# Kernel tuning notes

Measured on AMD Instinct MI355X. Metric: run time of the kernel, lower is better.

## Reference

```python
import jax, jax.numpy as jnp
import numpy as np

N = 100000   # nodes
E = 800000   # edges
P = 100000   # pos/neg pairs
H = 4        # heads
IN = 128     # input feature dim
HID = 32     # per-head out dim (H*HID = 128)


def gat_layer(h, src, dst, W, al, ar, b):
    """DGL-style GATConv: gather -> leaky_relu attention -> segment softmax -> scatter."""
    n = h.shape[0]
    nh, nf = al.shape
    feat = (h @ W).reshape(n, nh, nf)                       # [N,H,F]
    el = jnp.einsum('nhf,hf->nh', feat, al)                 # [N,H]
    er = jnp.einsum('nhf,hf->nh', feat, ar)                 # [N,H]
    e = jax.nn.leaky_relu(el[src] + er[dst], negative_slope=0.2)  # [E,H]
    emax = jax.ops.segment_max(e, dst, num_segments=n)      # [N,H]
    emax = jnp.where(jnp.isfinite(emax), emax, 0.0)         # zero-in-degree guard
    w = jnp.exp(e - emax[dst])                              # [E,H]
    denom = jax.ops.segment_sum(w, dst, num_segments=n)     # [N,H]
    alpha = w / jnp.maximum(denom[dst], 1e-9)               # [E,H]
    out = jax.ops.segment_sum(feat[src] * alpha[:, :, None], dst, num_segments=n)  # [N,H,F]
    return out.reshape(n, nh * nf) + b


def setup_inputs() -> dict:
    key = jax.random.key(0)
    ks = jax.random.split(key, 32)
    s = 0.1
    d = {
        'x': jax.random.normal(ks[0], (N, IN), jnp.float32),
        'src': jax.random.randint(ks[1], (E,), 0, N),
        'dst': jax.random.randint(ks[2], (E,), 0, N),
        'pos_src': jax.random.randint(ks[3], (P,), 0, N),
        'pos_dst': jax.random.randint(ks[4], (P,), 0, N),
        'neg_src': jax.random.randint(ks[5], (P,), 0, N),
        'neg_dst': jax.random.randint(ks[6], (P,), 0, N),
    }
    HF = H * HID
    # 3 GATConv layers, all 128 -> 4x32
    for l in range(3):
        ind = IN if l == 0 else HF
        d[f'W{l}'] = s * jax.random.normal(ks[7 + 4 * l], (ind, HF), jnp.float32)
        d[f'al{l}'] = s * jax.random.normal(ks[8 + 4 * l], (H, HID), jnp.float32)
        d[f'ar{l}'] = s * jax.random.normal(ks[9 + 4 * l], (H, HID), jnp.float32)
        d[f'b{l}'] = jnp.zeros((HF,), jnp.float32)
    # projection 128 -> 32
    d['Wp'] = s * jax.random.normal(ks[20], (HF, HID), jnp.float32)
    d['bp'] = jnp.zeros((HID,), jnp.float32)
    # predictor MLP 32 -> 32 -> 32 -> 1
    d['Wq1'] = s * jax.random.normal(ks[21], (HID, HID), jnp.float32)
    d['bq1'] = jnp.zeros((HID,), jnp.float32)
    d['Wq2'] = s * jax.random.normal(ks[22], (HID, HID), jnp.float32)
    d['bq2'] = jnp.zeros((HID,), jnp.float32)
    d['Wq3'] = s * jax.random.normal(ks[23], (HID, 1), jnp.float32)
    d['bq3'] = jnp.zeros((1,), jnp.float32)
    return d


def reference(x, src, dst, pos_src, pos_dst, neg_src, neg_dst,
              W0, al0, ar0, b0, W1, al1, ar1, b1, W2, al2, ar2, b2,
              Wp, bp, Wq1, bq1, Wq2, bq2, Wq3, bq3):
    h = x
    for W, al, ar, b in ((W0, al0, ar0, b0), (W1, al1, ar1, b1), (W2, al2, ar2, b2)):
        h = jax.nn.elu(gat_layer(h, src, dst, W, al, ar, b))
    h = h @ Wp + bp                                          # [N,HID]

    def predictor(z):
        z = jax.nn.relu(z @ Wq1 + bq1)
        z = jax.nn.relu(z @ Wq2 + bq2)
        return z @ Wq3 + bq3

    h_pos = predictor(h[pos_src] * h[pos_dst])               # [P,1]
    h_neg = predictor(h[neg_src] * h[neg_dst])               # [P,1]
    return (h_pos, h_neg)
```

## Files before the change

kernel.cpp:

```cpp
#include <hip/hip_runtime.h>
#include <math.h>

typedef __attribute__((ext_vector_type(8))) short bf16x8;
typedef __attribute__((ext_vector_type(4))) float f32x4;

__device__ __forceinline__ unsigned short f2bf_rtne(float v) {
    unsigned u = __float_as_uint(v);
    u += 0x7FFFu + ((u >> 16) & 1u);
    return (unsigned short)(u >> 16);
}

__global__ __launch_bounds__(256) void hist_k(const int* __restrict__ dst, int* __restrict__ deg, int e) {
    int i = blockIdx.x * 256 + threadIdx.x;
    if (i < e) atomicAdd(&deg[dst[i]], 1);
}

__global__ __launch_bounds__(256) void scan1_k(const int* __restrict__ deg, int* __restrict__ rowptr,
                                               int* __restrict__ bsum, int n) {
    __shared__ int sh[256];
    int tid = threadIdx.x;
    int sid = blockIdx.x * 256 + tid;
    int v = (sid < n) ? deg[sid] : 0;
    sh[tid] = v; __syncthreads();
    for (int off = 1; off < 256; off <<= 1) {
        int t = (tid >= off) ? sh[tid - off] : 0;
        __syncthreads();
        sh[tid] += t;
        __syncthreads();
    }
    if (sid < n) rowptr[sid + 1] = sh[tid];
    if (tid == 255) bsum[blockIdx.x] = sh[255];
}

__global__ __launch_bounds__(512) void scan2_k(int* __restrict__ bsum, int nb) {
    __shared__ int sh[512];
    int tid = threadIdx.x;
    sh[tid] = (tid < nb) ? bsum[tid] : 0;
    __syncthreads();
    for (int off = 1; off < 512; off <<= 1) {
        int t = (tid >= off) ? sh[tid - off] : 0;
        __syncthreads();
        sh[tid] += t;
        __syncthreads();
    }
    if (tid < nb) bsum[tid] = sh[tid];
}

__global__ __launch_bounds__(256) void scan3_k(int* __restrict__ rowptr, const int* __restrict__ bsum, int n) {
    int sid = blockIdx.x * 256 + threadIdx.x;
    if (sid == 0) rowptr[0] = 0;
    if (sid < n && blockIdx.x > 0) rowptr[sid + 1] += bsum[blockIdx.x - 1];
}

__global__ __launch_bounds__(256) void fill_k(const int* __restrict__ src, const int* __restrict__ dst,
                                              const int* __restrict__ rowptr, int* __restrict__ cursor,
                                              int* __restrict__ csrc, int* __restrict__ cdst, int e) {
    int i = blockIdx.x * 256 + threadIdx.x;
    if (i < e) {
        int d = dst[i];
        int pos = rowptr[d] + atomicAdd(&cursor[d], 1);
        csrc[pos] = src[i];
        cdst[pos] = d;
    }
}

__global__ __launch_bounds__(256) void wconv_k(const float* __restrict__ W, unsigned short* __restrict__ Bp) {
    int idx = blockIdx.x * 256 + threadIdx.x;
    int k = idx >> 7, nc = idx & 127;
    float v = W[idx];
    unsigned short h = f2bf_rtne(v);
    float hf = __uint_as_float((unsigned)h << 16);
    unsigned short lo = f2bf_rtne(v - hf);
    int n = nc >> 4, l15 = nc & 15, ks = k >> 5, lhi = (k >> 3) & 3, j = k & 7;
    int lanei = lhi * 16 + l15;
    Bp[(((ks * 16 + 2 * n) * 64) + lanei) * 8 + j] = h;
    Bp[(((ks * 16 + 2 * n + 1) * 64) + lanei) * 8 + j] = lo;
}

__global__ __launch_bounds__(256) void gemm_mfma_k(const float* __restrict__ A,
        const unsigned short* __restrict__ Bp,
        const float* __restrict__ alp, const float* __restrict__ arp,
        float* __restrict__ C, float* __restrict__ el, float* __restrict__ er, int M) {
    __shared__ short Bs[4][16][64][8];
    int tid = threadIdx.x;
    int wv = tid >> 6, lane = tid & 63;
    int l15 = lane & 15, lhi = lane >> 4;
    int mb = blockIdx.x * 128 + wv * 32;

    {
        const float4* g = (const float4*)Bp;
        float4* s = (float4*)&Bs[0][0][0][0];
        #pragma unroll
        for (int p = 0; p < 16; p++) s[tid + p * 256] = g[tid + p * 256];
    }

    const float* a0p = A + (size_t)min(mb + l15, M - 1) * 128 + lhi * 8;
    const float* a1p = A + (size_t)min(mb + 16 + l15, M - 1) * 128 + lhi * 8;
    float4 A0[4][2], A1[4][2];
    #pragma unroll
    for (int ks = 0; ks < 4; ks++) {
        A0[ks][0] = *(const float4*)(a0p + ks * 32);
        A0[ks][1] = *(const float4*)(a0p + ks * 32 + 4);
        A1[ks][0] = *(const float4*)(a1p + ks * 32);
        A1[ks][1] = *(const float4*)(a1p + ks * 32 + 4);
    }

    f32x4 acc[2][8];
    #pragma unroll
    for (int f = 0; f < 2; f++)
        #pragma unroll
        for (int n = 0; n < 8; n++) acc[f][n] = (f32x4){0.f, 0.f, 0.f, 0.f};

    float alv[8], arv[8];
    #pragma unroll
    for (int n = 0; n < 8; n++) { alv[n] = alp[n * 16 + l15]; arv[n] = arp[n * 16 + l15]; }

    __syncthreads();

    #pragma unroll
    for (int ks = 0; ks < 4; ks++) {
        float av[8];
        bf16x8 a0h, a0l, a1h, a1l;
        *(float4*)(av)     = A0[ks][0];
        *(float4*)(av + 4) = A0[ks][1];
        #pragma unroll
        for (int j = 0; j < 8; j++) {
            unsigned short h = f2bf_rtne(av[j]);
            a0h[j] = (short)h;
            a0l[j] = (short)f2bf_rtne(av[j] - __uint_as_float((unsigned)h << 16));
        }
        *(float4*)(av)     = A1[ks][0];
        *(float4*)(av + 4) = A1[ks][1];
        #pragma unroll
        for (int j = 0; j < 8; j++) {
            unsigned short h = f2bf_rtne(av[j]);
            a1h[j] = (short)h;
            a1l[j] = (short)f2bf_rtne(av[j] - __uint_as_float((unsigned)h << 16));
        }
        const bf16x8* bsv = (const bf16x8*)&Bs[ks][0][0][0];
        #pragma unroll
        for (int n = 0; n < 8; n++) {
            bf16x8 bhv = bsv[(2 * n) * 64 + lane];
            bf16x8 blv = bsv[(2 * n + 1) * 64 + lane];
            acc[0][n] = __builtin_amdgcn_mfma_f32_16x16x32_bf16(a0h, bhv, acc[0][n], 0, 0, 0);
            acc[1][n] = __builtin_amdgcn_mfma_f32_16x16x32_bf16(a1h, bhv, acc[1][n], 0, 0, 0);
            acc[0][n] = __builtin_amdgcn_mfma_f32_16x16x32_bf16(a0l, bhv, acc[0][n], 0, 0, 0);
            acc[1][n] = __builtin_amdgcn_mfma_f32_16x16x32_bf16(a1l, bhv, acc[1][n], 0, 0, 0);
            acc[0][n] = __builtin_amdgcn_mfma_f32_16x16x32_bf16(a0h, blv, acc[0][n], 0, 0, 0);
            acc[1][n] = __builtin_amdgcn_mfma_f32_16x16x32_bf16(a1h, blv, acc[1][n], 0, 0, 0);
        }
    }

    #pragma unroll
    for (int f = 0; f < 2; f++) {
        #pragma unroll
        for (int i = 0; i < 4; i++) {
            int r = mb + f * 16 + lhi * 4 + i;
            bool ok = (r < M);
            if (ok) {
                #pragma unroll
                for (int n = 0; n < 8; n++)
                    C[(size_t)r * 128 + n * 16 + l15] = acc[f][n][i];
            }
            float ph[4], qh[4];
            #pragma unroll
            for (int h = 0; h < 4; h++) {
                ph[h] = acc[f][2 * h][i] * alv[2 * h] + acc[f][2 * h + 1][i] * alv[2 * h + 1];
                qh[h] = acc[f][2 * h][i] * arv[2 * h] + acc[f][2 * h + 1][i] * arv[2 * h + 1];
            }
            #pragma unroll
            for (int off = 1; off < 16; off <<= 1) {
                #pragma unroll
                for (int h = 0; h < 4; h++) {
                    ph[h] += __shfl_xor(ph[h], off);
                    qh[h] += __shfl_xor(qh[h], off);
                }
            }
            if (ok && l15 < 8) {
                if (l15 < 4) {
                    float v = (l15 == 0) ? ph[0] : (l15 == 1) ? ph[1] : (l15 == 2) ? ph[2] : ph[3];
                    el[(size_t)r * 4 + l15] = v;
                } else {
                    int h = l15 - 4;
                    float v = (h == 0) ? qh[0] : (h == 1) ? qh[1] : (h == 2) ? qh[2] : qh[3];
                    er[(size_t)r * 4 + h] = v;
                }
            }
        }
    }
}

__global__ __launch_bounds__(256) void edgew_k(const int* __restrict__ csrc, const int* __restrict__ cdst,
                                               const float* __restrict__ el, const float* __restrict__ er,
                                               float* __restrict__ wbuf, int e) {
    int p = blockIdx.x * 256 + threadIdx.x;
    if (p >= e) return;
    int s = csrc[p], d = cdst[p];
    float4 l4 = *(const float4*)(el + (size_t)s * 4);
    float4 r4 = *(const float4*)(er + (size_t)d * 4);
    float e0 = l4.x + r4.x, e1 = l4.y + r4.y, e2 = l4.z + r4.z, e3 = l4.w + r4.w;
    e0 = (e0 > 0.f) ? e0 : 0.2f * e0;
    e1 = (e1 > 0.f) ? e1 : 0.2f * e1;
    e2 = (e2 > 0.f) ? e2 : 0.2f * e2;
    e3 = (e3 > 0.f) ? e3 : 0.2f * e3;
    *(float4*)(wbuf + (size_t)p * 4) = make_float4(__expf(e0), __expf(e1), __expf(e2), __expf(e3));
}

__global__ __launch_bounds__(256) void aggregate_k(const float* __restrict__ feat, const float* __restrict__ wbuf,
                                                   const int* __restrict__ rowptr, const int* __restrict__ csrc,
                                                   const float* __restrict__ bias, float* __restrict__ out, int n) {
    int wid = threadIdx.x >> 6;
    int lane = threadIdx.x & 63;
    int node = blockIdx.x * 4 + wid;
    if (node >= n) return;
    int h = lane >> 4;
    int p0 = rowptr[node], p1 = rowptr[node + 1];
    float2 b2 = *(const float2*)(bias + lane * 2);
    float lsum = 0.f, a0 = 0.f, a1 = 0.f;
    int p = p0;
    for (; p + 4 <= p1; p += 4) {
        int s0 = csrc[p], s1 = csrc[p + 1], s2 = csrc[p + 2], s3 = csrc[p + 3];
        float w0 = wbuf[(size_t)p * 4 + h];
        float w1 = wbuf[(size_t)(p + 1) * 4 + h];
        float w2 = wbuf[(size_t)(p + 2) * 4 + h];
        float w3 = wbuf[(size_t)(p + 3) * 4 + h];
        float2 f0 = *(const float2*)(feat + (size_t)s0 * 128 + lane * 2);
        float2 f1 = *(const float2*)(feat + (size_t)s1 * 128 + lane * 2);
        float2 f2 = *(const float2*)(feat + (size_t)s2 * 128 + lane * 2);
        float2 f3 = *(const float2*)(feat + (size_t)s3 * 128 + lane * 2);
        lsum += (w0 + w1) + (w2 + w3);
        a0 += w0 * f0.x + w1 * f1.x + w2 * f2.x + w3 * f3.x;
        a1 += w0 * f0.y + w1 * f1.y + w2 * f2.y + w3 * f3.y;
    }
    for (; p < p1; ++p) {
        int s = csrc[p];
        float w = wbuf[(size_t)p * 4 + h];
        float2 f = *(const float2*)(feat + (size_t)s * 128 + lane * 2);
        lsum += w;
        a0 += w * f.x;
        a1 += w * f.y;
    }
    float inv = 1.f / fmaxf(lsum, 1e-9f);
    float v0 = a0 * inv + b2.x;
    float v1 = a1 * inv + b2.y;
    v0 = (v0 > 0.f) ? v0 : expm1f(v0);
    v1 = (v1 > 0.f) ? v1 : expm1f(v1);
    *(float2*)(out + (size_t)node * 128 + lane * 2) = make_float2(v0, v1);
}

__global__ __launch_bounds__(256) void proj_k(const float* __restrict__ h, const float* __restrict__ Wp,
                                              const float* __restrict__ bp, float* __restrict__ hp, int n) {
    __shared__ float Ws[128 * 32];
    __shared__ float Hs[32][132];
    int tid = threadIdx.x;
    for (int i = tid; i < 4096; i += 256) Ws[i] = Wp[i];
    int n0 = blockIdx.x * 32;
    for (int i = tid; i < 1024; i += 256) {
        int r = i >> 5, c4 = i & 31;
        int node = n0 + r;
        float4 v = (node < n) ? *(const float4*)(h + (size_t)node * 128 + c4 * 4)
                              : make_float4(0.f, 0.f, 0.f, 0.f);
        *(float4*)&Hs[r][c4 * 4] = v;
    }
    __syncthreads();
    int r = tid >> 3;
    int node = n0 + r;
    int j0 = (tid & 7) * 4;
    if (node < n) {
        float a0 = bp[j0], a1 = bp[j0 + 1], a2 = bp[j0 + 2], a3 = bp[j0 + 3];
        #pragma unroll
        for (int k = 0; k < 128; k++) {
            float av = Hs[r][k];
            float4 w = *(const float4*)&Ws[k * 32 + j0];
            a0 += av * w.x; a1 += av * w.y; a2 += av * w.z; a3 += av * w.w;
        }
        *(float4*)(hp + (size_t)node * 32 + j0) = make_float4(a0, a1, a2, a3);
    }
}

__global__ __launch_bounds__(256) void predictor_k(const float* __restrict__ hp,
                                                   const int* __restrict__ ps, const int* __restrict__ pd,
                                                   const int* __restrict__ ns, const int* __restrict__ nd,
                                                   const float* __restrict__ Wq1, const float* __restrict__ bq1,
                                                   const float* __restrict__ Wq2, const float* __restrict__ bq2,
                                                   const float* __restrict__ Wq3, const float* __restrict__ bq3,
                                                   float* __restrict__ out, int P) {
    __shared__ float w1[1024], w2[1024], w3[32], b1[32], b2[32];
    int tid = threadIdx.x;
    for (int i = tid; i < 1024; i += 256) { w1[i] = Wq1[i]; w2[i] = Wq2[i]; }
    if (tid < 32) { w3[tid] = Wq3[tid]; b1[tid] = bq1[tid]; b2[tid] = bq2[tid]; }
    __syncthreads();
    int gid = blockIdx.x * 256 + tid;
    if (gid >= 2 * P) return;
    int i = (gid < P) ? gid : gid - P;
    int a = (gid < P) ? ps[i] : ns[i];
    int b = (gid < P) ? pd[i] : nd[i];
    float z[32];
    const float4* ha = (const float4*)(hp + (size_t)a * 32);
    const float4* hb = (const float4*)(hp + (size_t)b * 32);
    #pragma unroll
    for (int q = 0; q < 8; q++) {
        float4 x = ha[q], y = hb[q];
        z[q * 4 + 0] = x.x * y.x; z[q * 4 + 1] = x.y * y.y;
        z[q * 4 + 2] = x.z * y.z; z[q * 4 + 3] = x.w * y.w;
    }
    float z1[32];
    #pragma unroll
    for (int j = 0; j < 32; j++) {
        float s = b1[j];
        #pragma unroll
        for (int k = 0; k < 32; k++) s += z[k] * w1[k * 32 + j];
        z1[j] = fmaxf(s, 0.f);
    }
    #pragma unroll
    for (int j = 0; j < 32; j++) {
        float s = b2[j];
        #pragma unroll
        for (int k = 0; k < 32; k++) s += z1[k] * w2[k * 32 + j];
        z[j] = fmaxf(s, 0.f);
    }
    float s3 = bq3[0];
    #pragma unroll
    for (int j = 0; j < 32; j++) s3 += z[j] * w3[j];
    out[gid] = s3;
}

extern "C" void kernel_launch(void* const* d_in, const int* in_sizes, int n_in,
                              void* d_out, int out_size, void* d_ws, size_t ws_size,
                              hipStream_t stream) {
    const float* x   = (const float*)d_in[0];
    const int* src   = (const int*)d_in[1];
    const int* dst   = (const int*)d_in[2];
    const int* psrc  = (const int*)d_in[3];
    const int* pdst  = (const int*)d_in[4];
    const int* nsrc  = (const int*)d_in[5];
    const int* ndst  = (const int*)d_in[6];
    const float* W[3]  = { (const float*)d_in[7],  (const float*)d_in[11], (const float*)d_in[15] };
    const float* al[3] = { (const float*)d_in[8],  (const float*)d_in[12], (const float*)d_in[16] };
    const float* ar[3] = { (const float*)d_in[9],  (const float*)d_in[13], (const float*)d_in[17] };
    const float* bb[3] = { (const float*)d_in[10], (const float*)d_in[14], (const float*)d_in[18] };
    const float* Wp  = (const float*)d_in[19];
    const float* bp  = (const float*)d_in[20];
    const float* Wq1 = (const float*)d_in[21];
    const float* bq1 = (const float*)d_in[22];
    const float* Wq2 = (const float*)d_in[23];
    const float* bq2 = (const float*)d_in[24];
    const float* Wq3 = (const float*)d_in[25];
    const float* bq3 = (const float*)d_in[26];
    float* out = (float*)d_out;

    const int N = in_sizes[0] / 128;
    const int E = in_sizes[1];
    const int P = in_sizes[3];

    size_t off = 0;
    auto alloc = [&](size_t bytes) {
        void* p = (char*)d_ws + off;
        off += (bytes + 255) & ~(size_t)255;
        return p;
    };
    float* bufF  = (float*)alloc((size_t)N * 128 * 4);
    float* bufH  = (float*)alloc((size_t)N * 128 * 4);
    float* elA   = (float*)alloc((size_t)N * 4 * 4);
    float* erA   = (float*)alloc((size_t)N * 4 * 4);
    float* hp    = (float*)alloc((size_t)N * 32 * 4);
    int* rowptr  = (int*)alloc((size_t)(N + 1) * 4);
    int* csrc    = (int*)alloc((size_t)E * 4);
    int* cdst    = (int*)alloc((size_t)E * 4);
    float* wbuf  = (float*)alloc((size_t)E * 4 * 4);
    int* deg     = (int*)alloc((size_t)N * 4);
    int* cursor  = (int*)alloc((size_t)N * 4);
    int* bsum    = (int*)alloc(1024 * 4);
    unsigned short* Bp = (unsigned short*)alloc(32768 * 2);
    (void)ws_size;

    const int NB_E = (E + 255) / 256;
    const int NB_N = (N + 255) / 256;

    hipMemsetAsync(deg, 0, (size_t)N * 4, stream);
    hipMemsetAsync(cursor, 0, (size_t)N * 4, stream);

    hist_k<<<NB_E, 256, 0, stream>>>(dst, deg, E);
    scan1_k<<<NB_N, 256, 0, stream>>>(deg, rowptr, bsum, N);
    scan2_k<<<1, 512, 0, stream>>>(bsum, NB_N);
    scan3_k<<<NB_N, 256, 0, stream>>>(rowptr, bsum, N);
    fill_k<<<NB_E, 256, 0, stream>>>(src, dst, rowptr, cursor, csrc, cdst, E);

    const int GEMM_B = (N + 127) / 128;
    const float* hin = x;
    for (int l = 0; l < 3; l++) {
        wconv_k<<<64, 256, 0, stream>>>(W[l], Bp);
        gemm_mfma_k<<<GEMM_B, 256, 0, stream>>>(hin, Bp, al[l], ar[l], bufF, elA, erA, N);
        edgew_k<<<NB_E, 256, 0, stream>>>(csrc, cdst, elA, erA, wbuf, E);
        aggregate_k<<<(N + 3) / 4, 256, 0, stream>>>(bufF, wbuf, rowptr, csrc, bb[l], bufH, N);
        hin = bufH;
    }
    proj_k<<<(N + 31) / 32, 256, 0, stream>>>(bufH, Wp, bp, hp, N);
    predictor_k<<<(2 * P + 255) / 256, 256, 0, stream>>>(hp, psrc, pdst, nsrc, ndst,
                                                         Wq1, bq1, Wq2, bq2, Wq3, bq3, out, P);
}
```

Before: 488.0 us.

## Fuse edge-weight computation into aggregation and weight conversion into GEMM

Removes the edgew_k kernel and its per-edge wbuf buffer: the aggregation kernel now gathers el[src] and uses er[node] to compute leaky-relu and exp inline. The bf16 hi/lo weight split moves from a separate wconv_k kernel into the GEMM prologue, so each block converts W itself. CSR construction drops the cdst array and the cursor memset by seeding cursor from the scan. This cuts launches and E-sized memory traffic, at the cost of redundant exp work per lane group and repeated weight conversion in every GEMM block.

```diff
diff --git a/kernel.cpp b/kernel.cpp
--- a/kernel.cpp
+++ b/kernel.cpp
@@ -46,39 +46,29 @@
     if (tid < nb) bsum[tid] = sh[tid];
 }
 
-__global__ __launch_bounds__(256) void scan3_k(int* __restrict__ rowptr, const int* __restrict__ bsum, int n) {
+__global__ __launch_bounds__(256) void scan3_k(int* __restrict__ rowptr, int* __restrict__ cursor,
+                                               const int* __restrict__ bsum, int n) {
     int sid = blockIdx.x * 256 + threadIdx.x;
-    if (sid == 0) rowptr[0] = 0;
-    if (sid < n && blockIdx.x > 0) rowptr[sid + 1] += bsum[blockIdx.x - 1];
+    if (sid == 0) { rowptr[0] = 0; cursor[0] = 0; }
+    if (sid < n) {
+        int v = rowptr[sid + 1];
+        if (blockIdx.x > 0) v += bsum[blockIdx.x - 1];
+        rowptr[sid + 1] = v;
+        cursor[sid + 1] = v;
+    }
 }
 
 __global__ __launch_bounds__(256) void fill_k(const int* __restrict__ src, const int* __restrict__ dst,
-                                              const int* __restrict__ rowptr, int* __restrict__ cursor,
-                                              int* __restrict__ csrc, int* __restrict__ cdst, int e) {
+                                              int* __restrict__ cursor, int* __restrict__ csrc, int e) {
     int i = blockIdx.x * 256 + threadIdx.x;
     if (i < e) {
-        int d = dst[i];
-        int pos = rowptr[d] + atomicAdd(&cursor[d], 1);
+        int pos = atomicAdd(&cursor[dst[i]], 1);
         csrc[pos] = src[i];
-        cdst[pos] = d;
-    }
-}
-
-__global__ __launch_bounds__(256) void wconv_k(const float* __restrict__ W, unsigned short* __restrict__ Bp) {
-    int idx = blockIdx.x * 256 + threadIdx.x;
-    int k = idx >> 7, nc = idx & 127;
-    float v = W[idx];
-    unsigned short h = f2bf_rtne(v);
-    float hf = __uint_as_float((unsigned)h << 16);
-    unsigned short lo = f2bf_rtne(v - hf);
-    int n = nc >> 4, l15 = nc & 15, ks = k >> 5, lhi = (k >> 3) & 3, j = k & 7;
-    int lanei = lhi * 16 + l15;
-    Bp[(((ks * 16 + 2 * n) * 64) + lanei) * 8 + j] = h;
-    Bp[(((ks * 16 + 2 * n + 1) * 64) + lanei) * 8 + j] = lo;
+    }
 }
 
 __global__ __launch_bounds__(256) void gemm_mfma_k(const float* __restrict__ A,
-        const unsigned short* __restrict__ Bp,
+        const float* __restrict__ Wg,
         const float* __restrict__ alp, const float* __restrict__ arp,
         float* __restrict__ C, float* __restrict__ el, float* __restrict__ er, int M) {
     __shared__ short Bs[4][16][64][8];
@@ -86,13 +76,6 @@
     int wv = tid >> 6, lane = tid & 63;
     int l15 = lane & 15, lhi = lane >> 4;
     int mb = blockIdx.x * 128 + wv * 32;
-
-    {
-        const float4* g = (const float4*)Bp;
-        float4* s = (float4*)&Bs[0][0][0][0];
-        #pragma unroll
-        for (int p = 0; p < 16; p++) s[tid + p * 256] = g[tid + p * 256];
-    }
 
     const float* a0p = A + (size_t)min(mb + l15, M - 1) * 128 + lhi * 8;
     const float* a1p = A + (size_t)min(mb + 16 + l15, M - 1) * 128 + lhi * 8;
@@ -103,6 +86,25 @@
         A0[ks][1] = *(const float4*)(a0p + ks * 32 + 4);
         A1[ks][0] = *(const float4*)(a1p + ks * 32);
         A1[ks][1] = *(const float4*)(a1p + ks * 32 + 4);
+    }
+
+    #pragma unroll
+    for (int i = 0; i < 8; i++) {
+        int o = tid + i * 256;
+        int grp = o >> 7, nc = o & 127;
+        float wv8[8];
+        #pragma unroll
+        for (int j = 0; j < 8; j++) wv8[j] = Wg[(8 * grp + j) * 128 + nc];
+        bf16x8 hi, lo;
+        #pragma unroll
+        for (int j = 0; j < 8; j++) {
+            unsigned short h = f2bf_rtne(wv8[j]);
+            hi[j] = (short)h;
+            lo[j] = (short)f2bf_rtne(wv8[j] - __uint_as_float((unsigned)h << 16));
+        }
+        int ks = grp >> 2, lh2 = grp & 3, n = nc >> 4, l = nc & 15;
+        *(bf16x8*)&Bs[ks][2 * n][lh2 * 16 + l][0] = hi;
+        *(bf16x8*)&Bs[ks][2 * n + 1][lh2 * 16 + l][0] = lo;
     }
 
     f32x4 acc[2][8];
@@ -190,51 +192,44 @@
     }
 }
 
-__global__ __launch_bounds__(256) void edgew_k(const int* __restrict__ csrc, const int* __restrict__ cdst,
-                                               const float* __restrict__ el, const float* __restrict__ er,
-                                               float* __restrict__ wbuf, int e) {
-    int p = blockIdx.x * 256 + threadIdx.x;
-    if (p >= e) return;
-    int s = csrc[p], d = cdst[p];
-    float4 l4 = *(const float4*)(el + (size_t)s * 4);
-    float4 r4 = *(const float4*)(er + (size_t)d * 4);
-    float e0 = l4.x + r4.x, e1 = l4.y + r4.y, e2 = l4.z + r4.z, e3 = l4.w + r4.w;
-    e0 = (e0 > 0.f) ? e0 : 0.2f * e0;
-    e1 = (e1 > 0.f) ? e1 : 0.2f * e1;
-    e2 = (e2 > 0.f) ? e2 : 0.2f * e2;
-    e3 = (e3 > 0.f) ? e3 : 0.2f * e3;
-    *(float4*)(wbuf + (size_t)p * 4) = make_float4(__expf(e0), __expf(e1), __expf(e2), __expf(e3));
-}
-
-__global__ __launch_bounds__(256) void aggregate_k(const float* __restrict__ feat, const float* __restrict__ wbuf,
-                                                   const int* __restrict__ rowptr, const int* __restrict__ csrc,
-                                                   const float* __restrict__ bias, float* __restrict__ out, int n) {
+__global__ __launch_bounds__(256) void aggregate_k(const float* __restrict__ feat, const float* __restrict__ el,
+                                                   const float* __restrict__ er, const int* __restrict__ rowptr,
+                                                   const int* __restrict__ csrc, const float* __restrict__ bias,
+                                                   float* __restrict__ out, int n) {
     int wid = threadIdx.x >> 6;
     int lane = threadIdx.x & 63;
     int node = blockIdx.x * 4 + wid;
     if (node >= n) return;
     int h = lane >> 4;
     int p0 = rowptr[node], p1 = rowptr[node + 1];
+    float erv = er[(size_t)node * 4 + h];
     float2 b2 = *(const float2*)(bias + lane * 2);
     float lsum = 0.f, a0 = 0.f, a1 = 0.f;
     int p = p0;
     for (; p + 4 <= p1; p += 4) {
         int s0 = csrc[p], s1 = csrc[p + 1], s2 = csrc[p + 2], s3 = csrc[p + 3];
-        float w0 = wbuf[(size_t)p * 4 + h];
-        float w1 = wbuf[(size_t)(p + 1) * 4 + h];
-        float w2 = wbuf[(size_t)(p + 2) * 4 + h];
-        float w3 = wbuf[(size_t)(p + 3) * 4 + h];
+        float e0 = el[(size_t)s0 * 4 + h] + erv;
+        float e1 = el[(size_t)s1 * 4 + h] + erv;
+        float e2 = el[(size_t)s2 * 4 + h] + erv;
+        float e3 = el[(size_t)s3 * 4 + h] + erv;
+        e0 = (e0 > 0.f) ? e0 : 0.2f * e0;
+        e1 = (e1 > 0.f) ? e1 : 0.2f * e1;
+        e2 = (e2 > 0.f) ? e2 : 0.2f * e2;
+        e3 = (e3 > 0.f) ? e3 : 0.2f * e3;
         float2 f0 = *(const float2*)(feat + (size_t)s0 * 128 + lane * 2);
         float2 f1 = *(const float2*)(feat + (size_t)s1 * 128 + lane * 2);
         float2 f2 = *(const float2*)(feat + (size_t)s2 * 128 + lane * 2);
         float2 f3 = *(const float2*)(feat + (size_t)s3 * 128 + lane * 2);
+        float w0 = __expf(e0), w1 = __expf(e1), w2 = __expf(e2), w3 = __expf(e3);
         lsum += (w0 + w1) + (w2 + w3);
         a0 += w0 * f0.x + w1 * f1.x + w2 * f2.x + w3 * f3.x;
         a1 += w0 * f0.y + w1 * f1.y + w2 * f2.y + w3 * f3.y;
     }
     for (; p < p1; ++p) {
         int s = csrc[p];
-        float w = wbuf[(size_t)p * 4 + h];
+        float e = el[(size_t)s * 4 + h] + erv;
+        e = (e > 0.f) ? e : 0.2f * e;
+        float w = __expf(e);
         float2 f = *(const float2*)(feat + (size_t)s * 128 + lane * 2);
         lsum += w;
         a0 += w * f.x;
@@ -365,34 +360,28 @@
     float* erA   = (float*)alloc((size_t)N * 4 * 4);
     float* hp    = (float*)alloc((size_t)N * 32 * 4);
     int* rowptr  = (int*)alloc((size_t)(N + 1) * 4);
+    int* cursor  = (int*)alloc((size_t)(N + 1) * 4);
     int* csrc    = (int*)alloc((size_t)E * 4);
-    int* cdst    = (int*)alloc((size_t)E * 4);
-    float* wbuf  = (float*)alloc((size_t)E * 4 * 4);
     int* deg     = (int*)alloc((size_t)N * 4);
-    int* cursor  = (int*)alloc((size_t)N * 4);
     int* bsum    = (int*)alloc(1024 * 4);
-    unsigned short* Bp = (unsigned short*)alloc(32768 * 2);
     (void)ws_size;
 
     const int NB_E = (E + 255) / 256;
     const int NB_N = (N + 255) / 256;
 
     hipMemsetAsync(deg, 0, (size_t)N * 4, stream);
-    hipMemsetAsync(cursor, 0, (size_t)N * 4, stream);
 
     hist_k<<<NB_E, 256, 0, stream>>>(dst, deg, E);
     scan1_k<<<NB_N, 256, 0, stream>>>(deg, rowptr, bsum, N);
     scan2_k<<<1, 512, 0, stream>>>(bsum, NB_N);
-    scan3_k<<<NB_N, 256, 0, stream>>>(rowptr, bsum, N);
-    fill_k<<<NB_E, 256, 0, stream>>>(src, dst, rowptr, cursor, csrc, cdst, E);
+    scan3_k<<<NB_N, 256, 0, stream>>>(rowptr, cursor, bsum, N);
+    fill_k<<<NB_E, 256, 0, stream>>>(src, dst, cursor, csrc, E);
 
     const int GEMM_B = (N + 127) / 128;
     const float* hin = x;
     for (int l = 0; l < 3; l++) {
-        wconv_k<<<64, 256, 0, stream>>>(W[l], Bp);
-        gemm_mfma_k<<<GEMM_B, 256, 0, stream>>>(hin, Bp, al[l], ar[l], bufF, elA, erA, N);
-        edgew_k<<<NB_E, 256, 0, stream>>>(csrc, cdst, elA, erA, wbuf, E);
-        aggregate_k<<<(N + 3) / 4, 256, 0, stream>>>(bufF, wbuf, rowptr, csrc, bb[l], bufH, N);
+        gemm_mfma_k<<<GEMM_B, 256, 0, stream>>>(hin, W[l], al[l], ar[l], bufF, elA, erA, N);
+        aggregate_k<<<(N + 3) / 4, 256, 0, stream>>>(bufF, elA, erA, rowptr, csrc, bb[l], bufH, N);
         hin = bufH;
     }
     proj_k<<<(N + 31) / 32, 256, 0, stream>>>(bufH, Wp, bp, hp, N);
```

After: 471.6 us. 3.4% less time.
